# Performance work log

Measured on AMD Instinct MI355X. Metric: run time of the kernel, lower is better.

Reference implementation:

```python
import jax, jax.numpy as jnp
import numpy as np

B, N_ELEC, N_NUC, F = 4096, 64, 16, 128
CUTOFF = 5.0  # hardcoded in original forward (radius(e, n, 5.0))


def setup_inputs() -> dict:
    key = jax.random.key(0)
    k1, k2, k3, k4 = jax.random.split(key, 4)
    return {
        "s_nuc": jax.random.normal(k1, (B, N_NUC, F), jnp.float32),
        "v_nuc": jax.random.normal(k2, (B, N_NUC, 3, F), jnp.float32),
        "coord_elec": jax.random.normal(k3, (B, N_ELEC, 3), jnp.float32) * 3.0,
        "coord_nuc": jax.random.normal(k4, (N_NUC, 3), jnp.float32) * 3.0,
    }


def reference(s_nuc, v_nuc, coord_elec, coord_nuc):
    # Per-sample bipartite radius graph nuc->elec, then PyG-style batching
    # (node indices offset by n_nuc / n_elec per graph). Since jit requires
    # static shapes, we emit the dense set of all (nuc, elec) pairs plus a
    # boolean mask marking edges within the cutoff radius.
    b_dim, n_elec = coord_elec.shape[:2]
    n_nuc = coord_nuc.shape[0]
    f = s_nuc.shape[-1]

    # diff[b, i, j, :] = coord_elec[b, j] - coord_nuc[i]  (== elec[col] - nuc[row])
    diff = coord_elec[:, None, :, :] - coord_nuc[None, :, None, :]  # [B, n_nuc, n_elec, 3]
    dist = jnp.linalg.norm(diff, axis=-1)                            # [B, n_nuc, n_elec]
    mask = (dist < CUTOFF).reshape(-1)                               # [B*n_nuc*n_elec]

    bidx = jnp.arange(b_dim)[:, None, None]
    row = bidx * n_nuc + jnp.arange(n_nuc)[None, :, None]   # nuc index (batched)
    col = bidx * n_elec + jnp.arange(n_elec)[None, None, :]  # elec index (batched)
    row = jnp.broadcast_to(row, (b_dim, n_nuc, n_elec)).reshape(-1)
    col = jnp.broadcast_to(col, (b_dim, n_nuc, n_elec)).reshape(-1)
    edge_index = jnp.stack([row, col])                        # [2, B*n_nuc*n_elec]

    edge_attr = diff.reshape(-1, 3)
    s_flat = s_nuc.reshape(b_dim * n_nuc, f)
    v_flat = v_nuc.reshape(b_dim * n_nuc, 3, f)
    return (s_flat, v_flat, edge_index, edge_attr, mask)
```

## Files before the change

### kernel.cpp

```cpp
#include <hip/hip_runtime.h>
#include <math.h>

#define BB 4096
#define N_ELEC 64
#define N_NUC 16
#define FF 128
#define CUTOFF 5.0f

static constexpr long long S_SIZE = (long long)BB * N_NUC * FF;
static constexpr long long V_SIZE = (long long)BB * N_NUC * 3 * FF;
static constexpr long long E_CNT  = (long long)BB * N_NUC * N_ELEC;

static constexpr long long OFF_S  = 0;
static constexpr long long OFF_V  = OFF_S + S_SIZE;
static constexpr long long OFF_EI = OFF_V + V_SIZE;
static constexpr long long OFF_EA = OFF_EI + 2 * E_CNT;
static constexpr long long OFF_M  = OFF_EA + 3 * E_CNT;

__global__ __launch_bounds__(256) void copy_sv_kernel(
    const float4* __restrict__ s, const float4* __restrict__ v,
    float4* __restrict__ out) {
    constexpr long long S4 = S_SIZE / 4;
    constexpr long long V4 = V_SIZE / 4;
    long long i = (long long)blockIdx.x * blockDim.x + threadIdx.x;
    if (i >= S4 + V4) return;
    out[i] = (i < S4) ? s[i] : v[i - S4];
}

__global__ __launch_bounds__(256) void edge_kernel(
    const float* __restrict__ coord_elec,
    const float* __restrict__ coord_nuc,
    float* __restrict__ out) {
    __shared__ float nuc[N_NUC * 3];
    if (threadIdx.x < N_NUC * 3) nuc[threadIdx.x] = coord_nuc[threadIdx.x];
    __syncthreads();

    long long e = (long long)blockIdx.x * blockDim.x + threadIdx.x;
    if (e >= E_CNT) return;

    int b = (int)(e >> 10);
    int i = (int)((e >> 6) & 15);
    int j = (int)(e & 63);

    const float* ep = coord_elec + ((long long)b * N_ELEC + j) * 3;
    float d0 = ep[0] - nuc[i * 3 + 0];
    float d1 = ep[1] - nuc[i * 3 + 1];
    float d2 = ep[2] - nuc[i * 3 + 2];

    long long ea = OFF_EA + e * 3;
    out[ea + 0] = d0;
    out[ea + 1] = d1;
    out[ea + 2] = d2;

    out[OFF_EI + e]         = (float)(b * N_NUC + i);
    out[OFF_EI + E_CNT + e] = (float)(b * N_ELEC + j);

    float dist = sqrtf(d0 * d0 + d1 * d1 + d2 * d2);
    out[OFF_M + e] = (dist < CUTOFF) ? 1.0f : 0.0f;
}

extern "C" void kernel_launch(void* const* d_in, const int* in_sizes, int n_in,
                              void* d_out, int out_size, void* d_ws, size_t ws_size,
                              hipStream_t stream) {
    const float* s_nuc      = (const float*)d_in[0];
    const float* v_nuc      = (const float*)d_in[1];
    const float* coord_elec = (const float*)d_in[2];
    const float* coord_nuc  = (const float*)d_in[3];
    float* out = (float*)d_out;

    constexpr long long TOT4 = (S_SIZE + V_SIZE) / 4;
    int copy_blocks = (int)((TOT4 + 255) / 256);
    copy_sv_kernel<<<copy_blocks, 256, 0, stream>>>(
        (const float4*)s_nuc, (const float4*)v_nuc, (float4*)out);

    int edge_blocks = (int)((E_CNT + 255) / 256);
    edge_kernel<<<edge_blocks, 256, 0, stream>>>(coord_elec, coord_nuc, out);
}
```

Before: 334.4 us.

## Fuse copy and edge kernels, stage edge attrs in LDS, use nontemporal stores

Merges the s/v copy and the edge generation into a single launch, with the block index selecting the role. Electron coordinates are staged in shared memory, and each block's edge_attr tile is staged in LDS so it can be written with coalesced 16-byte vector stores instead of strided 3-float stores. Loads and stores use nontemporal builtins so the large streaming traffic does not pollute the caches. The costs are an extra barrier per edge block, more LDS use, and branch divergence between the block roles.

After: 319.7 us. 4.4% less time.

```diff
diff --git a/kernel.cpp b/kernel.cpp
--- a/kernel.cpp
+++ b/kernel.cpp
@@ -7,56 +7,72 @@
 #define FF 128
 #define CUTOFF 5.0f
 
+typedef float v4f __attribute__((ext_vector_type(4)));
+
 static constexpr long long S_SIZE = (long long)BB * N_NUC * FF;
 static constexpr long long V_SIZE = (long long)BB * N_NUC * 3 * FF;
 static constexpr long long E_CNT  = (long long)BB * N_NUC * N_ELEC;
 
-static constexpr long long OFF_S  = 0;
-static constexpr long long OFF_V  = OFF_S + S_SIZE;
-static constexpr long long OFF_EI = OFF_V + V_SIZE;
+static constexpr long long OFF_EI = S_SIZE + V_SIZE;
 static constexpr long long OFF_EA = OFF_EI + 2 * E_CNT;
 static constexpr long long OFF_M  = OFF_EA + 3 * E_CNT;
 
-__global__ __launch_bounds__(256) void copy_sv_kernel(
-    const float4* __restrict__ s, const float4* __restrict__ v,
-    float4* __restrict__ out) {
-    constexpr long long S4 = S_SIZE / 4;
-    constexpr long long V4 = V_SIZE / 4;
-    long long i = (long long)blockIdx.x * blockDim.x + threadIdx.x;
-    if (i >= S4 + V4) return;
-    out[i] = (i < S4) ? s[i] : v[i - S4];
-}
+static constexpr int COPY_BLOCKS = (int)((S_SIZE + V_SIZE) / 4 / 256);
+static constexpr int EDGE_BLOCKS = (int)(E_CNT / 256);
 
-__global__ __launch_bounds__(256) void edge_kernel(
+__global__ __launch_bounds__(256) void fused_kernel(
+    const v4f* __restrict__ s, const v4f* __restrict__ v,
     const float* __restrict__ coord_elec,
     const float* __restrict__ coord_nuc,
-    float* __restrict__ out) {
+    float* __restrict__ out)
+{
+    const int bid = blockIdx.x;
+    const int t = threadIdx.x;
+
+    if (bid < COPY_BLOCKS) {
+        long long i = (long long)bid * 256 + t;
+        constexpr long long S4 = S_SIZE / 4;
+        v4f val = (i < S4) ? __builtin_nontemporal_load(&s[i])
+                           : __builtin_nontemporal_load(&v[i - S4]);
+        __builtin_nontemporal_store(val, &((v4f*)out)[i]);
+        return;
+    }
+
     __shared__ float nuc[N_NUC * 3];
-    if (threadIdx.x < N_NUC * 3) nuc[threadIdx.x] = coord_nuc[threadIdx.x];
+    __shared__ float elec[N_ELEC * 3];
+    __shared__ float attr[256 * 3];
+
+    const long long e0 = (long long)(bid - COPY_BLOCKS) * 256;
+    const int b = (int)(e0 >> 10);
+
+    if (t < 48) nuc[t] = coord_nuc[t];
+    if (t >= 64 && t < 64 + 192)
+        elec[t - 64] = coord_elec[(long long)b * (N_ELEC * 3) + (t - 64)];
     __syncthreads();
 
-    long long e = (long long)blockIdx.x * blockDim.x + threadIdx.x;
-    if (e >= E_CNT) return;
+    const long long e = e0 + t;
+    const int i = (int)((e >> 6) & 15);
+    const int j = t & 63;
 
-    int b = (int)(e >> 10);
-    int i = (int)((e >> 6) & 15);
-    int j = (int)(e & 63);
+    float d0 = elec[j * 3 + 0] - nuc[i * 3 + 0];
+    float d1 = elec[j * 3 + 1] - nuc[i * 3 + 1];
+    float d2 = elec[j * 3 + 2] - nuc[i * 3 + 2];
 
-    const float* ep = coord_elec + ((long long)b * N_ELEC + j) * 3;
-    float d0 = ep[0] - nuc[i * 3 + 0];
-    float d1 = ep[1] - nuc[i * 3 + 1];
-    float d2 = ep[2] - nuc[i * 3 + 2];
+    attr[t * 3 + 0] = d0;
+    attr[t * 3 + 1] = d1;
+    attr[t * 3 + 2] = d2;
 
-    long long ea = OFF_EA + e * 3;
-    out[ea + 0] = d0;
-    out[ea + 1] = d1;
-    out[ea + 2] = d2;
+    __builtin_nontemporal_store((float)(b * N_NUC + i),  &out[OFF_EI + e]);
+    __builtin_nontemporal_store((float)(b * N_ELEC + j), &out[OFF_EI + E_CNT + e]);
+    float dist = sqrtf(d0 * d0 + d1 * d1 + d2 * d2);
+    __builtin_nontemporal_store(dist < CUTOFF ? 1.0f : 0.0f, &out[OFF_M + e]);
 
-    out[OFF_EI + e]         = (float)(b * N_NUC + i);
-    out[OFF_EI + E_CNT + e] = (float)(b * N_ELEC + j);
+    __syncthreads();
 
-    float dist = sqrtf(d0 * d0 + d1 * d1 + d2 * d2);
-    out[OFF_M + e] = (dist < CUTOFF) ? 1.0f : 0.0f;
+    if (t < 192) {
+        v4f* dst = (v4f*)(out + OFF_EA + e0 * 3);
+        __builtin_nontemporal_store(((const v4f*)attr)[t], &dst[t]);
+    }
 }
 
 extern "C" void kernel_launch(void* const* d_in, const int* in_sizes, int n_in,
@@ -68,11 +84,6 @@
     const float* coord_nuc  = (const float*)d_in[3];
     float* out = (float*)d_out;
 
-    constexpr long long TOT4 = (S_SIZE + V_SIZE) / 4;
-    int copy_blocks = (int)((TOT4 + 255) / 256);
-    copy_sv_kernel<<<copy_blocks, 256, 0, stream>>>(
-        (const float4*)s_nuc, (const float4*)v_nuc, (float4*)out);
-
-    int edge_blocks = (int)((E_CNT + 255) / 256);
-    edge_kernel<<<edge_blocks, 256, 0, stream>>>(coord_elec, coord_nuc, out);
+    fused_kernel<<<COPY_BLOCKS + EDGE_BLOCKS, 256, 0, stream>>>(
+        (const v4f*)s_nuc, (const v4f*)v_nuc, coord_elec, coord_nuc, out);
 }
```
